# Optimization experiments

Measured on AMD Instinct MI355X. Metric: run time of the kernel, lower is better.

Reference implementation:

```python
import jax, jax.numpy as jnp
import numpy as np

PASSES = 5
NUM_EDGE_SETS = 3
B, N, D = 8, 20000, 128
E = 64000
HID, OUT = 80, 10


def setup_inputs() -> dict:
    key = jax.random.key(0)
    ks = jax.random.split(key, 8)
    nodes = jax.random.normal(ks[0], (B, N, D), dtype=jnp.float32)
    problem_type = jax.random.normal(ks[1], (B, 1), dtype=jnp.float32)
    # edges[b, k, e] = (dst, src); index_add target is column 0, gathered source is column 1
    edges = jax.random.randint(ks[2], (B, NUM_EDGE_SETS, E, 2), 0, N, dtype=jnp.int32)
    w1 = jax.random.normal(ks[3], (D + 1, HID), jnp.float32) / np.sqrt(D + 1).astype(np.float32)
    b1 = jnp.zeros((HID,), jnp.float32)
    w2 = jax.random.normal(ks[4], (HID, HID), jnp.float32) / np.sqrt(HID).astype(np.float32)
    b2 = jnp.zeros((HID,), jnp.float32)
    w3 = jax.random.normal(ks[5], (HID, OUT), jnp.float32) / np.sqrt(HID).astype(np.float32)
    b3 = jnp.zeros((OUT,), jnp.float32)
    return {"nodes": nodes, "problem_type": problem_type, "w1": w1, "b1": b1,
            "w2": w2, "b2": b2, "w3": w3, "b3": b3, "edges": edges}


def _message_pass(nodes_g, edges_g):
    # nodes_g: [N, D]; edges_g: [K, E, 2] with (dst, src)
    inc = jnp.zeros_like(nodes_g)
    for k in range(NUM_EDGE_SETS):  # small fixed set of edge types
        dst = edges_g[k, :, 0]
        src = edges_g[k, :, 1]
        inc = inc + jax.ops.segment_sum(nodes_g[src], dst, num_segments=N)
    return nodes_g + inc


def _forward(nodes, problem_type, w1, b1, w2, b2, w3, b3, edges):
    step = jax.vmap(_message_pass)  # over batch of graphs

    def body(n, _):
        return step(n, edges), None

    nodes, _ = jax.lax.scan(body, nodes, None, length=PASSES)
    pooled = nodes.sum(axis=1)                       # [B, D]
    y = jnp.log(pooled)
    y = jnp.where(jnp.isnan(y), 0.0, y)              # nan -> 0
    y = jax.nn.relu(y)
    finite_max = jnp.max(jnp.where(jnp.isinf(y), -jnp.inf, y), axis=1, keepdims=True)
    y = jnp.where(y == jnp.inf, finite_max, y)       # +inf -> max finite entry
    x = jnp.concatenate([y, problem_type], axis=1)   # [B, D+1]
    x = jax.nn.leaky_relu(x @ w1 + b1)
    x = jax.nn.leaky_relu(x @ w2 + b2)
    return x @ w3 + b3                               # [B, OUT]


def reference(nodes, problem_type, w1, b1, w2, b2, w3, b3, edges):
    return _forward(nodes, problem_type, w1, b1, w2, b2, w3, b3, edges)
```

## Files before the change

kernel.cpp:

```cpp
#include <hip/hip_runtime.h>
#include <cmath>

#define NB 8
#define NN 20000
#define ND 128
#define NE_TOT 192000

#define RSZ 128
#define NR 157
#define CAP 2048
#define ECHUNK 8000
#define NCHUNK 24

#define GR 5
#define NCG 32

__device__ float g_w0[NB * NN];
__device__ float g_w1[NB * NN];
__device__ int   g_bcnt[NB][NCHUNK][NR];
__device__ int   g_cnt[NB * NR];
__device__ int2  g_bucket[(size_t)NB * NR * CAP];
__device__ float g_ppart[NB * NCG * ND];

__global__ void initCountK(const int* __restrict__ edges) {
    __shared__ int hist[NR];
    const int b = blockIdx.x / NCHUNK, c = blockIdx.x % NCHUNK;
    const int t = threadIdx.x;

    for (int i = blockIdx.x * 256 + t; i < NB * NN; i += NB * NCHUNK * 256)
        g_w0[i] = 1.0f;

    for (int i = t; i < NR; i += 256) hist[i] = 0;
    __syncthreads();
    const int2* __restrict__ ep =
        (const int2*)edges + (size_t)b * NE_TOT + (size_t)c * ECHUNK;
    for (int i = t; i < ECHUNK; i += 256)
        atomicAdd(&hist[ep[i].y >> 7], 1);
    __syncthreads();
    for (int i = t; i < NR; i += 256) g_bcnt[b][c][i] = hist[i];
}

__global__ void distK(const int* __restrict__ edges) {
    __shared__ int cur[NR];
    const int b = blockIdx.x / NCHUNK, c = blockIdx.x % NCHUNK;
    const int t = threadIdx.x;
    for (int r = t; r < NR; r += 256) {
        int off = 0;
        for (int cc = 0; cc < c; ++cc) off += g_bcnt[b][cc][r];
        cur[r] = off;
        if (c == NCHUNK - 1) g_cnt[b * NR + r] = off + g_bcnt[b][c][r];
    }
    __syncthreads();
    const int2* __restrict__ ep =
        (const int2*)edges + (size_t)b * NE_TOT + (size_t)c * ECHUNK;
    for (int i = t; i < ECHUNK; i += 256) {
        const int2 e = ep[i];
        const int r = e.y >> 7;
        const int pos = atomicAdd(&cur[r], 1);
        if (pos < CAP)
            g_bucket[((size_t)b * NR + r) * CAP + pos] = make_int2(e.x, e.y & (RSZ - 1));
    }
}

__global__ void __launch_bounds__(1024)
passLDSK(int sel) {
    extern __shared__ float w_lds[];
    __shared__ float acc[GR * RSZ];
    const int b  = blockIdx.y;
    const int r0 = blockIdx.x * GR;
    const int gr = min(GR, NR - r0);
    const int t  = threadIdx.x;
    const float* __restrict__ w  = sel ? g_w1 : g_w0;
    float* __restrict__ wn       = sel ? g_w0 : g_w1;
    const float* __restrict__ wb = w + b * NN;

    const float4* __restrict__ wb4 = (const float4*)wb;
    for (int i = t; i < NN / 4; i += 1024) ((float4*)w_lds)[i] = wb4[i];
    if (t < GR * RSZ) acc[t] = 0.0f;
    __syncthreads();

    for (int rr = 0; rr < gr; ++rr) {
        const int u = b * NR + r0 + rr;
        const int cnt = g_cnt[u];
        const int2* __restrict__ bk = g_bucket + (size_t)u * CAP;
        float* accr = acc + rr * RSZ;
        for (int i = t; i < cnt; i += 1024) {
            const int2 e = bk[i];
            unsafeAtomicAdd(&accr[e.y], w_lds[e.x]);
        }
    }
    __syncthreads();

    for (int i = t; i < gr * RSZ; i += 1024) {
        const int node = r0 * RSZ + i;
        if (node < NN) wn[b * NN + node] = w_lds[node] + acc[i];
    }
}

__global__ void __launch_bounds__(1024)
pass5poolK(const float* __restrict__ nodes) {
    extern __shared__ float w_lds[];
    __shared__ float acc[GR * RSZ];
    __shared__ float w5s[GR * RSZ];
    const int b  = blockIdx.y;
    const int r0 = blockIdx.x * GR;
    const int gr = min(GR, NR - r0);
    const int t  = threadIdx.x;
    const float* __restrict__ wb = g_w0 + b * NN;

    const float4* __restrict__ wb4 = (const float4*)wb;
    for (int i = t; i < NN / 4; i += 1024) ((float4*)w_lds)[i] = wb4[i];
    if (t < GR * RSZ) acc[t] = 0.0f;
    __syncthreads();

    for (int rr = 0; rr < gr; ++rr) {
        const int u = b * NR + r0 + rr;
        const int cnt = g_cnt[u];
        const int2* __restrict__ bk = g_bucket + (size_t)u * CAP;
        float* accr = acc + rr * RSZ;
        for (int i = t; i < cnt; i += 1024) {
            const int2 e = bk[i];
            unsafeAtomicAdd(&accr[e.y], w_lds[e.x]);
        }
    }
    __syncthreads();

    if (t < GR * RSZ) {
        const int node = r0 * RSZ + t;
        w5s[t] = (t < gr * RSZ && node < NN) ? w_lds[node] + acc[t] : 0.0f;
    }
    __syncthreads();

    const int dslot = t & 31, rg = t >> 5;
    const int nbase = r0 * RSZ;
    const int nrows = min(GR * RSZ, NN - nbase);
    const float4* __restrict__ base = (const float4*)(nodes + (size_t)b * NN * ND);
    float4 aA = {0.f, 0.f, 0.f, 0.f}, aB = {0.f, 0.f, 0.f, 0.f};
    int row = rg;
    for (; row + 32 < nrows; row += 64) {
        const float wA = w5s[row], wB = w5s[row + 32];
        const float4 vA = base[(size_t)(nbase + row) * 32 + dslot];
        const float4 vB = base[(size_t)(nbase + row + 32) * 32 + dslot];
        aA.x += wA * vA.x; aA.y += wA * vA.y; aA.z += wA * vA.z; aA.w += wA * vA.w;
        aB.x += wB * vB.x; aB.y += wB * vB.y; aB.z += wB * vB.z; aB.w += wB * vB.w;
    }
    if (row < nrows) {
        const float wA = w5s[row];
        const float4 vA = base[(size_t)(nbase + row) * 32 + dslot];
        aA.x += wA * vA.x; aA.y += wA * vA.y; aA.z += wA * vA.z; aA.w += wA * vA.w;
    }
    float4 s4;
    s4.x = aA.x + aB.x; s4.y = aA.y + aB.y; s4.z = aA.z + aB.z; s4.w = aA.w + aB.w;

    __syncthreads();
    float4* red = (float4*)w_lds;
    red[t] = s4;
    __syncthreads();
    if (t < 32) {
        float4 s = red[t];
        for (int g = 1; g < 32; ++g) {
            const float4 o = red[g * 32 + t];
            s.x += o.x; s.y += o.y; s.z += o.z; s.w += o.w;
        }
        ((float4*)g_ppart)[((size_t)b * NCG + blockIdx.x) * 32 + t] = s;
    }
}

__global__ void reduceHeadK(const float* __restrict__ ptype,
                            const float* __restrict__ w1, const float* __restrict__ b1,
                            const float* __restrict__ w2, const float* __restrict__ b2,
                            const float* __restrict__ w3, const float* __restrict__ b3,
                            float* __restrict__ out) {
    __shared__ float sx[NB][ND + 1];
    __shared__ float h1s[NB][80];
    __shared__ float h2s[NB][80];
    const int t = threadIdx.x;
    const int b = t >> 7, d = t & 127;

    float s = 0.0f;
    for (int j = 0; j < NCG; ++j)
        s += g_ppart[(b * NCG + j) * ND + d];

    float y = logf(s);
    if (isnan(y)) y = 0.0f;
    y = fmaxf(y, 0.0f);
    sx[b][d] = y;
    __syncthreads();

    if (t < NB) {
        float fm = -INFINITY;
        for (int dd = 0; dd < ND; ++dd) {
            const float v = sx[t][dd];
            if (!isinf(v)) fm = fmaxf(fm, v);
        }
        for (int dd = 0; dd < ND; ++dd)
            if (isinf(sx[t][dd])) sx[t][dd] = fm;
        sx[t][ND] = ptype[t];
    }
    __syncthreads();

    if (t < NB * 80) {
        const int bb = t / 80, j = t - bb * 80;
        float v = b1[j];
        for (int k = 0; k < ND + 1; ++k) v += sx[bb][k] * w1[k * 80 + j];
        h1s[bb][j] = v > 0.0f ? v : 0.01f * v;
    }
    __syncthreads();

    if (t < NB * 80) {
        const int bb = t / 80, j = t - bb * 80;
        float v = b2[j];
        for (int k = 0; k < 80; ++k) v += h1s[bb][k] * w2[k * 80 + j];
        h2s[bb][j] = v > 0.0f ? v : 0.01f * v;
    }
    __syncthreads();

    if (t < NB * 10) {
        const int bb = t / 10, j = t - bb * 10;
        float v = b3[j];
        for (int k = 0; k < 80; ++k) v += h2s[bb][k] * w3[k * 10 + j];
        out[bb * 10 + j] = v;
    }
}

extern "C" void kernel_launch(void* const* d_in, const int* in_sizes, int n_in,
                              void* d_out, int out_size, void* d_ws, size_t ws_size,
                              hipStream_t stream) {
    const float* nodes = (const float*)d_in[0];
    const float* ptype = (const float*)d_in[1];
    const float* w1    = (const float*)d_in[2];
    const float* b1    = (const float*)d_in[3];
    const float* w2    = (const float*)d_in[4];
    const float* b2    = (const float*)d_in[5];
    const float* w3    = (const float*)d_in[6];
    const float* b3    = (const float*)d_in[7];
    const int*   edges = (const int*)d_in[8];
    float* out = (float*)d_out;

    initCountK<<<NB * NCHUNK, 256, 0, stream>>>(edges);
    distK<<<NB * NCHUNK, 256, 0, stream>>>(edges);

    passLDSK<<<dim3(NCG, NB), 1024, NN * sizeof(float), stream>>>(0);
    passLDSK<<<dim3(NCG, NB), 1024, NN * sizeof(float), stream>>>(1);
    passLDSK<<<dim3(NCG, NB), 1024, NN * sizeof(float), stream>>>(0);
    passLDSK<<<dim3(NCG, NB), 1024, NN * sizeof(float), stream>>>(1);

    pass5poolK<<<dim3(NCG, NB), 1024, NN * sizeof(float), stream>>>(nodes);

    reduceHeadK<<<1, 1024, 0, stream>>>(ptype, w1, b1, w2, b2, w3, b3, out);
}
```

Measured before the change: 129.7 us.

## Use one 640-node bucket per block with register-prefetched edges and a specialized first pass

Replaces the 128-node row buckets with 32 buckets of 640 nodes, so each block owns exactly one bucket with a fixed capacity of 8192 edges. Each thread loads its 8 edges into registers before the LDS weight fill, so edge fetch latency overlaps the weight load. The first pass is templated to treat all weights as 1, which skips the weight initialization in the count kernel and the per-block copy of the weight vector into LDS. In exchange, each thread always loads 8 bucket slots even past the edge count, and correctness relies on no bucket exceeding 8192 edges.

After: 130.1 us. Within noise of the previous version (+0.4%).

```diff
diff --git a/kernel.cpp b/kernel.cpp
--- a/kernel.cpp
+++ b/kernel.cpp
@@ -6,134 +6,128 @@
 #define ND 128
 #define NE_TOT 192000
 
-#define RSZ 128
-#define NR 157
-#define CAP 2048
+#define GSZ 640
+#define NG 32
+#define FIX 8192
+#define KPT 8
 #define ECHUNK 8000
 #define NCHUNK 24
 
-#define GR 5
-#define NCG 32
-
 __device__ float g_w0[NB * NN];
 __device__ float g_w1[NB * NN];
-__device__ int   g_bcnt[NB][NCHUNK][NR];
-__device__ int   g_cnt[NB * NR];
-__device__ int2  g_bucket[(size_t)NB * NR * CAP];
-__device__ float g_ppart[NB * NCG * ND];
-
-__global__ void initCountK(const int* __restrict__ edges) {
-    __shared__ int hist[NR];
+__device__ int   g_bcnt[NB][NCHUNK][NG];
+__device__ int   g_cnt[NB * NG];
+__device__ int2  g_bucket[(size_t)NB * NG * FIX];
+__device__ float g_ppart[NB * NG * ND];
+
+__global__ void countK(const int* __restrict__ edges) {
+    __shared__ int hist[NG];
     const int b = blockIdx.x / NCHUNK, c = blockIdx.x % NCHUNK;
     const int t = threadIdx.x;
-
-    for (int i = blockIdx.x * 256 + t; i < NB * NN; i += NB * NCHUNK * 256)
-        g_w0[i] = 1.0f;
-
-    for (int i = t; i < NR; i += 256) hist[i] = 0;
+    if (t < NG) hist[t] = 0;
     __syncthreads();
     const int2* __restrict__ ep =
         (const int2*)edges + (size_t)b * NE_TOT + (size_t)c * ECHUNK;
     for (int i = t; i < ECHUNK; i += 256)
-        atomicAdd(&hist[ep[i].y >> 7], 1);
-    __syncthreads();
-    for (int i = t; i < NR; i += 256) g_bcnt[b][c][i] = hist[i];
+        atomicAdd(&hist[(unsigned)ep[i].y / GSZ], 1);
+    __syncthreads();
+    if (t < NG) g_bcnt[b][c][t] = hist[t];
 }
 
 __global__ void distK(const int* __restrict__ edges) {
-    __shared__ int cur[NR];
+    __shared__ int cur[NG];
     const int b = blockIdx.x / NCHUNK, c = blockIdx.x % NCHUNK;
     const int t = threadIdx.x;
-    for (int r = t; r < NR; r += 256) {
+    if (t < NG) {
         int off = 0;
-        for (int cc = 0; cc < c; ++cc) off += g_bcnt[b][cc][r];
-        cur[r] = off;
-        if (c == NCHUNK - 1) g_cnt[b * NR + r] = off + g_bcnt[b][c][r];
+        for (int cc = 0; cc < c; ++cc) off += g_bcnt[b][cc][t];
+        cur[t] = off;
+        if (c == NCHUNK - 1) g_cnt[b * NG + t] = off + g_bcnt[b][c][t];
     }
     __syncthreads();
     const int2* __restrict__ ep =
         (const int2*)edges + (size_t)b * NE_TOT + (size_t)c * ECHUNK;
     for (int i = t; i < ECHUNK; i += 256) {
         const int2 e = ep[i];
-        const int r = e.y >> 7;
-        const int pos = atomicAdd(&cur[r], 1);
-        if (pos < CAP)
-            g_bucket[((size_t)b * NR + r) * CAP + pos] = make_int2(e.x, e.y & (RSZ - 1));
-    }
-}
-
+        const unsigned g = (unsigned)e.y / GSZ;
+        const int pos = atomicAdd(&cur[g], 1);
+        if (pos < FIX)
+            g_bucket[((size_t)(b * NG + g)) * FIX + pos] =
+                make_int2(e.x, e.y - (int)g * GSZ);
+    }
+}
+
+template<bool FIRST>
 __global__ void __launch_bounds__(1024)
-passLDSK(int sel) {
+passK(int sel) {
     extern __shared__ float w_lds[];
-    __shared__ float acc[GR * RSZ];
-    const int b  = blockIdx.y;
-    const int r0 = blockIdx.x * GR;
-    const int gr = min(GR, NR - r0);
-    const int t  = threadIdx.x;
-    const float* __restrict__ w  = sel ? g_w1 : g_w0;
-    float* __restrict__ wn       = sel ? g_w0 : g_w1;
-    const float* __restrict__ wb = w + b * NN;
-
-    const float4* __restrict__ wb4 = (const float4*)wb;
-    for (int i = t; i < NN / 4; i += 1024) ((float4*)w_lds)[i] = wb4[i];
-    if (t < GR * RSZ) acc[t] = 0.0f;
-    __syncthreads();
-
-    for (int rr = 0; rr < gr; ++rr) {
-        const int u = b * NR + r0 + rr;
-        const int cnt = g_cnt[u];
-        const int2* __restrict__ bk = g_bucket + (size_t)u * CAP;
-        float* accr = acc + rr * RSZ;
-        for (int i = t; i < cnt; i += 1024) {
-            const int2 e = bk[i];
-            unsafeAtomicAdd(&accr[e.y], w_lds[e.x]);
-        }
-    }
-    __syncthreads();
-
-    for (int i = t; i < gr * RSZ; i += 1024) {
-        const int node = r0 * RSZ + i;
-        if (node < NN) wn[b * NN + node] = w_lds[node] + acc[i];
+    __shared__ float acc[GSZ + 8];
+    const int b = blockIdx.y, g = blockIdx.x;
+    const int t = threadIdx.x;
+    const float* __restrict__ wb = (sel ? g_w1 : g_w0) + b * NN;
+    float* __restrict__ wn       = (sel ? g_w0 : g_w1) + b * NN;
+    const int cnt = g_cnt[b * NG + g];
+    const int2* __restrict__ bk = g_bucket + (size_t)(b * NG + g) * FIX + t;
+
+    int2 e[KPT];
+#pragma unroll
+    for (int k = 0; k < KPT; ++k) e[k] = bk[k * 1024];
+
+    if (!FIRST) {
+        const float4* __restrict__ wb4 = (const float4*)wb;
+        for (int i = t; i < NN / 4; i += 1024) ((float4*)w_lds)[i] = wb4[i];
+    }
+    if (t < GSZ + 8) acc[t] = 0.0f;
+    __syncthreads();
+
+#pragma unroll
+    for (int k = 0; k < KPT; ++k)
+        if (k * 1024 + t < cnt)
+            unsafeAtomicAdd(&acc[e[k].y], FIRST ? 1.0f : w_lds[e[k].x]);
+    __syncthreads();
+
+    if (t < GSZ) {
+        const int node = g * GSZ + t;
+        if (node < NN)
+            wn[node] = (FIRST ? 1.0f : w_lds[node]) + acc[t];
     }
 }
 
 __global__ void __launch_bounds__(1024)
 pass5poolK(const float* __restrict__ nodes) {
     extern __shared__ float w_lds[];
-    __shared__ float acc[GR * RSZ];
-    __shared__ float w5s[GR * RSZ];
-    const int b  = blockIdx.y;
-    const int r0 = blockIdx.x * GR;
-    const int gr = min(GR, NR - r0);
-    const int t  = threadIdx.x;
+    __shared__ float acc[GSZ + 8];
+    __shared__ float w5s[GSZ];
+    const int b = blockIdx.y, g = blockIdx.x;
+    const int t = threadIdx.x;
     const float* __restrict__ wb = g_w0 + b * NN;
+    const int cnt = g_cnt[b * NG + g];
+    const int2* __restrict__ bk = g_bucket + (size_t)(b * NG + g) * FIX + t;
+
+    int2 e[KPT];
+#pragma unroll
+    for (int k = 0; k < KPT; ++k) e[k] = bk[k * 1024];
 
     const float4* __restrict__ wb4 = (const float4*)wb;
     for (int i = t; i < NN / 4; i += 1024) ((float4*)w_lds)[i] = wb4[i];
-    if (t < GR * RSZ) acc[t] = 0.0f;
-    __syncthreads();
-
-    for (int rr = 0; rr < gr; ++rr) {
-        const int u = b * NR + r0 + rr;
-        const int cnt = g_cnt[u];
-        const int2* __restrict__ bk = g_bucket + (size_t)u * CAP;
-        float* accr = acc + rr * RSZ;
-        for (int i = t; i < cnt; i += 1024) {
-            const int2 e = bk[i];
-            unsafeAtomicAdd(&accr[e.y], w_lds[e.x]);
-        }
-    }
-    __syncthreads();
-
-    if (t < GR * RSZ) {
-        const int node = r0 * RSZ + t;
-        w5s[t] = (t < gr * RSZ && node < NN) ? w_lds[node] + acc[t] : 0.0f;
+    if (t < GSZ + 8) acc[t] = 0.0f;
+    __syncthreads();
+
+#pragma unroll
+    for (int k = 0; k < KPT; ++k)
+        if (k * 1024 + t < cnt)
+            unsafeAtomicAdd(&acc[e[k].y], w_lds[e[k].x]);
+    __syncthreads();
+
+    if (t < GSZ) {
+        const int node = g * GSZ + t;
+        w5s[t] = (node < NN) ? w_lds[node] + acc[t] : 0.0f;
     }
     __syncthreads();
 
     const int dslot = t & 31, rg = t >> 5;
-    const int nbase = r0 * RSZ;
-    const int nrows = min(GR * RSZ, NN - nbase);
+    const int nbase = g * GSZ;
+    const int nrows = min(GSZ, NN - nbase);
     const float4* __restrict__ base = (const float4*)(nodes + (size_t)b * NN * ND);
     float4 aA = {0.f, 0.f, 0.f, 0.f}, aB = {0.f, 0.f, 0.f, 0.f};
     int row = rg;
@@ -158,11 +152,11 @@
     __syncthreads();
     if (t < 32) {
         float4 s = red[t];
-        for (int g = 1; g < 32; ++g) {
-            const float4 o = red[g * 32 + t];
+        for (int q = 1; q < 32; ++q) {
+            const float4 o = red[q * 32 + t];
             s.x += o.x; s.y += o.y; s.z += o.z; s.w += o.w;
         }
-        ((float4*)g_ppart)[((size_t)b * NCG + blockIdx.x) * 32 + t] = s;
+        ((float4*)g_ppart)[((size_t)b * NG + g) * 32 + t] = s;
     }
 }
 
@@ -178,8 +172,8 @@
     const int b = t >> 7, d = t & 127;
 
     float s = 0.0f;
-    for (int j = 0; j < NCG; ++j)
-        s += g_ppart[(b * NCG + j) * ND + d];
+    for (int j = 0; j < NG; ++j)
+        s += g_ppart[(b * NG + j) * ND + d];
 
     float y = logf(s);
     if (isnan(y)) y = 0.0f;
@@ -237,15 +231,15 @@
     const int*   edges = (const int*)d_in[8];
     float* out = (float*)d_out;
 
-    initCountK<<<NB * NCHUNK, 256, 0, stream>>>(edges);
+    countK<<<NB * NCHUNK, 256, 0, stream>>>(edges);
     distK<<<NB * NCHUNK, 256, 0, stream>>>(edges);
 
-    passLDSK<<<dim3(NCG, NB), 1024, NN * sizeof(float), stream>>>(0);
-    passLDSK<<<dim3(NCG, NB), 1024, NN * sizeof(float), stream>>>(1);
-    passLDSK<<<dim3(NCG, NB), 1024, NN * sizeof(float), stream>>>(0);
-    passLDSK<<<dim3(NCG, NB), 1024, NN * sizeof(float), stream>>>(1);
-
-    pass5poolK<<<dim3(NCG, NB), 1024, NN * sizeof(float), stream>>>(nodes);
+    passK<true><<<dim3(NG, NB), 1024, 0, stream>>>(0);
+    passK<false><<<dim3(NG, NB), 1024, NN * sizeof(float), stream>>>(1);
+    passK<false><<<dim3(NG, NB), 1024, NN * sizeof(float), stream>>>(0);
+    passK<false><<<dim3(NG, NB), 1024, NN * sizeof(float), stream>>>(1);
+
+    pass5poolK<<<dim3(NG, NB), 1024, NN * sizeof(float), stream>>>(nodes);
 
     reduceHeadK<<<1, 1024, 0, stream>>>(ptype, w1, b1, w2, b2, w3, b3, out);
 }
```
